# Kernel tuning notes

Hardware: AMD Instinct MI355X
Metric: run time of the kernel (lower is better)

Reference implementation:

```python
import jax, jax.numpy as jnp
import numpy as np
from jax import lax

BN_EPS = 1e-5


def _bn(t, g, b, m, v):
    # eval-mode BatchNorm2d over channel axis 1
    scale = (g / jnp.sqrt(v + BN_EPS))[None, :, None, None]
    return (t - m[None, :, None, None]) * scale + b[None, :, None, None]


def _conv1x1(t, w):
    # w: (out_c, in_c)
    return jnp.einsum('bchw,oc->bohw', t, w)


def setup_inputs() -> dict:
    key = jax.random.key(0)
    ks = jax.random.split(key, 8)
    B, C_in, H, W = 16, 640, 32, 32
    x = jax.random.normal(ks[0], (B, C_in, H, W), dtype=jnp.float32)

    def bn_params(k, c):
        k1, k2, k3, k4 = jax.random.split(k, 4)
        return (jax.random.normal(k1, (c,), jnp.float32) * 0.1 + 1.0,  # gamma
                jax.random.normal(k2, (c,), jnp.float32) * 0.1,        # beta
                jax.random.normal(k3, (c,), jnp.float32) * 0.1,        # running mean
                jax.random.uniform(k4, (c,), jnp.float32) + 0.5)       # running var

    bn1_g, bn1_b, bn1_m, bn1_v = bn_params(ks[1], 640)
    w_in = jax.random.normal(ks[2], (64, 640), jnp.float32) / np.sqrt(640)
    bnin_g, bnin_b, bnin_m, bnin_v = bn_params(ks[3], 64)
    w_emb = jax.random.normal(ks[4], (640, 1664), jnp.float32) / np.sqrt(1664)
    bne_g, bne_b, bne_m, bne_v = bn_params(ks[5], 640)
    w_out = jax.random.normal(ks[6], (640, 640), jnp.float32) / np.sqrt(640)
    bno_g, bno_b, bno_m, bno_v = bn_params(ks[7], 640)

    return dict(x=x,
                bn1_g=bn1_g, bn1_b=bn1_b, bn1_m=bn1_m, bn1_v=bn1_v,
                w_in=w_in, bnin_g=bnin_g, bnin_b=bnin_b, bnin_m=bnin_m, bnin_v=bnin_v,
                w_emb=w_emb, bne_g=bne_g, bne_b=bne_b, bne_m=bne_m, bne_v=bne_v,
                w_out=w_out, bno_g=bno_g, bno_b=bno_b, bno_m=bno_m, bno_v=bno_v)


def reference(x,
              bn1_g, bn1_b, bn1_m, bn1_v,
              w_in, bnin_g, bnin_b, bnin_m, bnin_v,
              w_emb, bne_g, bne_b, bne_m, bne_v,
              w_out, bno_g, bno_b, bno_m, bno_v):
    KH, KW = 5, 5
    x = jax.nn.relu(_bn(x, bn1_g, bn1_b, bn1_m, bn1_v))
    x = jax.nn.relu(_bn(_conv1x1(x, w_in), bnin_g, bnin_b, bnin_m, bnin_v))
    x0 = jax.nn.relu(x)  # second ReLU in original forward (no-op but faithful)
    # F.normalize(x, dim=1, p=2), eps=1e-12 (PyTorch default)
    norm = jnp.sqrt(jnp.sum(x0 * x0, axis=1, keepdims=True))
    identity = x0 / jnp.maximum(norm, 1e-12)
    b, c, h, w = identity.shape
    # unfold: (b, c*KH*KW, h, w), channel-major ordering matches torch Unfold
    patches = lax.conv_general_dilated_patches(
        identity, (KH, KW), (1, 1), ((2, 2), (2, 2)))
    corr = patches.reshape(b, c, KH * KW, h, w) * identity[:, :, None, :, :]
    corr = corr.reshape(b, c * KH * KW, h, w)
    # featureL2Norm: sqrt(sum(x^2, 1) + 1e-6)
    gs = corr / jnp.sqrt(jnp.sum(corr * corr, axis=1, keepdims=True) + 1e-6)
    feat = jnp.concatenate([identity, gs], axis=1)  # (b, 1664, h, w)
    e = jax.nn.relu(_bn(_conv1x1(feat, w_emb), bne_g, bne_b, bne_m, bne_v))
    out = _bn(_conv1x1(e, w_out), bno_g, bno_b, bno_m, bno_v)
    # dropout in eval mode = identity
    return out
```

## Files before the change

### kernel.cpp

```cpp
#include <hip/hip_runtime.h>
#include <math.h>

#define BN_EPS 1e-5f

using short8  = __attribute__((ext_vector_type(8))) short;
using f32x16  = __attribute__((ext_vector_type(16))) float;


__device__ __forceinline__ float bflo(unsigned u) { return __uint_as_float(u << 16); }
__device__ __forceinline__ float bfhi(unsigned u) { return __uint_as_float(u & 0xffff0000u); }

__device__ __forceinline__ unsigned bf16_rne(float f) {
    unsigned u = __float_as_uint(f);
    return (u + 0x7fffu + ((u >> 16) & 1u)) >> 16;
}
__device__ __forceinline__ unsigned pack_bf16(float lo, float hi) {
    return bf16_rne(lo) | (bf16_rne(hi) << 16);
}
__device__ __forceinline__ unsigned pk_hu(float lo, float hi) {
    unsigned a = __float_as_uint(lo) + 0x8000u;
    unsigned b = __float_as_uint(hi) + 0x8000u;
    return __builtin_amdgcn_perm(b, a, 0x07060302u);
}
__device__ __forceinline__ unsigned pmul_fast(unsigned a, unsigned b) {
    return pk_hu(bflo(a) * bflo(b), bfhi(a) * bfhi(b));
}

__global__ __launch_bounds__(256)
void k_prepAll(const float* __restrict__ g1, const float* __restrict__ b1,
               const float* __restrict__ m1, const float* __restrict__ v1,
               const float* __restrict__ w_in,
               const float* __restrict__ gi, const float* __restrict__ bi,
               const float* __restrict__ mi, const float* __restrict__ vi,
               const float* __restrict__ w_emb,
               const float* __restrict__ ge, const float* __restrict__ be,
               const float* __restrict__ me, const float* __restrict__ ve,
               const float* __restrict__ w_out,
               const float* __restrict__ go, const float* __restrict__ bo,
               const float* __restrict__ mo, const float* __restrict__ vo,
               float* __restrict__ s1, float* __restrict__ b1c,
               float* __restrict__ biasI, float* __restrict__ biasE, float* __restrict__ biasO,
               unsigned* __restrict__ wIt, unsigned* __restrict__ wEt, unsigned* __restrict__ wOt)
{
    __shared__ float row[1664];
    const int tid = threadIdx.x;

    if (blockIdx.x < 640) {
        const int oc = blockIdx.x;
#pragma unroll
        for (int it = 0; it < 2; it++) {
            int u = it * 256 + tid;
            if (u < 416)
                ((float4*)row)[u] = ((const float4*)&w_emb[(size_t)oc * 1664])[u];
        }
        __syncthreads();
        if (tid < 208) {
            int kc = tid >> 2, kh = (tid >> 1) & 1, ksub = tid & 1;
            int k0 = kc * 32 + kh * 16 + ksub * 8;
            float sc = ge[oc] * rsqrtf(ve[oc] + BN_EPS);
            float v[8];
#pragma unroll
            for (int j = 0; j < 8; j++) {
                int kgp = k0 + j;
                int orig;
                if (kgp < 64) orig = kgp;
                else { int t = kgp - 64; orig = 64 + (t & 63) * 25 + (t >> 6); }
                v[j] = row[orig] * sc;
            }
            int mt = oc >> 7, mf = (oc >> 5) & 3;
            int idx = (mt * 52 + kc) * 512 + (mf * 2 + kh) * 64 + ksub * 32 + (oc & 31);
            ((uint4*)wEt)[idx] = make_uint4(pack_bf16(v[0], v[1]), pack_bf16(v[2], v[3]),
                                            pack_bf16(v[4], v[5]), pack_bf16(v[6], v[7]));
        }
        return;
    }

    int i = (blockIdx.x - 640) * 256 + tid;

    if (i < 640) {
        float s = g1[i] * rsqrtf(v1[i] + BN_EPS);
        s1[i] = s; b1c[i] = b1[i] - m1[i] * s;
    } else if (i < 704) {
        int c = i - 640;
        float s = gi[c] * rsqrtf(vi[c] + BN_EPS);
        biasI[c] = bi[c] - mi[c] * s;
    } else if (i < 1344) {
        int c = i - 704;
        float s = ge[c] * rsqrtf(ve[c] + BN_EPS);
        biasE[c] = be[c] - me[c] * s;
    } else if (i < 1984) {
        int c = i - 1344;
        float s = go[c] * rsqrtf(vo[c] + BN_EPS);
        biasO[c] = bo[c] - mo[c] * s;
    }

    if (i >= 2048 && i < 7168) {
        int u = i - 2048;
        int kc = u >> 8, w = u & 255;
        int mf = w >> 7, kh = (w >> 6) & 1, sl = w & 63;
        int oc = mf * 32 + (sl & 31);
        int k0 = kc * 32 + kh * 16 + (sl >> 5) * 8;
        float sc = gi[oc] * rsqrtf(vi[oc] + BN_EPS);
        unsigned d[4];
#pragma unroll
        for (int q = 0; q < 4; q++)
            d[q] = pack_bf16(w_in[oc * 640 + k0 + 2 * q] * sc,
                             w_in[oc * 640 + k0 + 2 * q + 1] * sc);
        ((uint4*)wIt)[u] = make_uint4(d[0], d[1], d[2], d[3]);
    }

    if (i >= 8192 && i < 59392) {
        int u = i - 8192;
        int ci = u >> 9, w = u & 511;
        int mt = ci / 20, kc = ci - mt * 20;
        int mf = w >> 7, kh = (w >> 6) & 1, sl = w & 63;
        int oc = mt * 128 + mf * 32 + (sl & 31);
        int k0 = kc * 32 + kh * 16 + (sl >> 5) * 8;
        float sc = go[oc] * rsqrtf(vo[oc] + BN_EPS);
        unsigned d[4];
#pragma unroll
        for (int q = 0; q < 4; q++)
            d[q] = pack_bf16(w_out[oc * 640 + k0 + 2 * q] * sc,
                             w_out[oc * 640 + k0 + 2 * q + 1] * sc);
        ((uint4*)wOt)[u] = make_uint4(d[0], d[1], d[2], d[3]);
    }
}

__global__ __launch_bounds__(512, 1)
void k_identity(const float* __restrict__ x,
                const float* __restrict__ s1, const float* __restrict__ b1c,
                const unsigned* __restrict__ wIt, const float* __restrict__ biasI,
                unsigned* __restrict__ ident)
{
    __shared__ short smem[2][4096];
    __shared__ float Tpart[64 * 65];
    __shared__ float T[64 * 68];
    __shared__ float inv[64];

    const int tid  = threadIdx.x;
    const int half = tid >> 8;
    const int t    = tid & 255;
    const int l = t & 63, wv = t >> 6;
    const int mf = wv >> 1, nf = wv & 1;
    const int p0 = blockIdx.x * 64;
    const int b = p0 >> 10, hw0 = p0 & 1023;

    f32x16 acc;
#pragma unroll
    for (int r = 0; r < 16; r++) acc[r] = 0.f;

    for (int i = 0; i < 10; i++) {
        const int kc = half * 10 + i;
        uint4 av = ((const uint4*)wIt)[kc * 256 + t];
        int bnf = t >> 7, bkh = (t >> 6) & 1, sl = t & 63;
        int px = bnf * 32 + (sl & 31);
        int ch0 = kc * 32 + bkh * 16 + (sl >> 5) * 8;
        float4 sA = *(const float4*)&s1[ch0], sB = *(const float4*)&s1[ch0 + 4];
        float4 bA = *(const float4*)&b1c[ch0], bB = *(const float4*)&b1c[ch0 + 4];
        float vv[8];
        const float* xp = &x[((size_t)b * 640 + ch0) * 1024 + hw0 + px];
        vv[0] = fmaxf(fmaf(xp[0], sA.x, bA.x), 0.f);
        vv[1] = fmaxf(fmaf(xp[1024], sA.y, bA.y), 0.f);
        vv[2] = fmaxf(fmaf(xp[2048], sA.z, bA.z), 0.f);
        vv[3] = fmaxf(fmaf(xp[3072], sA.w, bA.w), 0.f);
        vv[4] = fmaxf(fmaf(xp[4096], sB.x, bB.x), 0.f);
        vv[5] = fmaxf(fmaf(xp[5120], sB.y, bB.y), 0.f);
        vv[6] = fmaxf(fmaf(xp[6144], sB.z, bB.z), 0.f);
        vv[7] = fmaxf(fmaf(xp[7168], sB.w, bB.w), 0.f);
        uint4 bvpk = make_uint4(pack_bf16(vv[0], vv[1]), pack_bf16(vv[2], vv[3]),
                                pack_bf16(vv[4], vv[5]), pack_bf16(vv[6], vv[7]));
        __syncthreads();
        ((uint4*)smem[half])[t] = av;
        ((uint4*)(smem[half] + 2048))[t] = bvpk;
        __syncthreads();
#pragma unroll
        for (int kh = 0; kh < 2; kh++) {
            short8 a  = *(const short8*)&smem[half][((mf * 2 + kh) * 64 + l) * 8];
            short8 bb = *(const short8*)&smem[half][2048 + ((nf * 2 + kh) * 64 + l) * 8];
            acc = __builtin_amdgcn_mfma_f32_32x32x16_bf16(a, bb, acc, 0, 0, 0);
        }
    }
    if (half == 1) {
#pragma unroll
        for (int r = 0; r < 16; r++) {
            int m = mf * 32 + (r & 3) + 8 * (r >> 2) + 4 * (l >> 5);
            int px = nf * 32 + (l & 31);
            Tpart[px * 65 + m] = acc[r];
        }
    }
    __syncthreads();
    if (half == 0) {
#pragma unroll
        for (int r = 0; r < 16; r++) {
            int m = mf * 32 + (r & 3) + 8 * (r >> 2) + 4 * (l >> 5);
            int px = nf * 32 + (l & 31);
            float v = acc[r] + Tpart[px * 65 + m];
            T[px * 68 + m] = fmaxf(v + biasI[m], 0.f);
        }
    }
    __syncthreads();
    if (tid < 64) {
        float sum = 0.f;
#pragma unroll 8
        for (int c = 0; c < 64; c++) { float v = T[tid * 68 + c]; sum = fmaf(v, v, sum); }
        inv[tid] = 1.f / fmaxf(sqrtf(sum), 1e-12f);
    }
    __syncthreads();
    {
        int px = tid >> 3, q = tid & 7;
        float iv = inv[px];
        unsigned d[4];
#pragma unroll
        for (int t2 = 0; t2 < 4; t2++)
            d[t2] = pack_bf16(T[px * 68 + q * 8 + 2 * t2] * iv,
                              T[px * 68 + q * 8 + 2 * t2 + 1] * iv);
        *(uint4*)&ident[(size_t)(p0 + px) * 32 + q * 4] = make_uint4(d[0], d[1], d[2], d[3]);
    }
}

#define FS_SLAB 0
#define FS_CTRS 15552
__global__ __launch_bounds__(512, 1)
void k_feat(const unsigned* __restrict__ ident, unsigned* __restrict__ featC, int ptBase)
{
    __shared__ short smem[20160];
    __shared__ float invDs[64];

    const int tid = threadIdx.x;
    const int pt = ptBase + blockIdx.x;
    const int b = pt >> 4, r0 = (pt & 15) * 2;

#pragma unroll
    for (int it = 0; it < 4; it++) {
        int u = it * 512 + tid;
        if (u < 1728) {
            int spx = u >> 3, q = u & 7;
            int sr = spx / 36, sc = spx - sr * 36;
            int r = r0 + sr - 2, c = sc - 2;
            uint4 v = make_uint4(0u, 0u, 0u, 0u);
            if (r >= 0 && r < 32 && c >= 0 && c < 32)
                v = *(const uint4*)&ident[((size_t)(b * 1024 + r * 32 + c) * 64 + q * 8) / 2];
            *(uint4*)&smem[FS_SLAB + spx * 72 + q * 8] = v;
        }
    }
    __syncthreads();

    {
        int px = tid >> 3, part = tid & 7;
        int rh = px >> 5, rw = px & 31;
        float ctr[8];
        const unsigned* cp = (const unsigned*)&smem[FS_SLAB + ((rh + 2) * 36 + rw + 2) * 72 + part * 8];
#pragma unroll
        for (int d = 0; d < 4; d++) { ctr[2 * d] = bflo(cp[d]); ctr[2 * d + 1] = bfhi(cp[d]); }
        float sum = 0.f;
#pragma unroll
        for (int k = 0; k < 25; k++) {
            const int kh = k / 5, kw = k % 5;
            const unsigned* nb = (const unsigned*)&smem[FS_SLAB + ((rh + kh) * 36 + rw + kw) * 72 + part * 8];
#pragma unroll
            for (int d = 0; d < 4; d++) {
                float q0 = bflo(nb[d]) * ctr[2 * d];
                float q1 = bfhi(nb[d]) * ctr[2 * d + 1];
                sum = fmaf(q0, q0, sum); sum = fmaf(q1, q1, sum);
            }
        }
        sum += __shfl_xor(sum, 1);
        sum += __shfl_xor(sum, 2);
        sum += __shfl_xor(sum, 4);
        if (part == 0) invDs[px] = rsqrtf(sum + 1e-6f);
    }
    __syncthreads();

    {
        int px = tid >> 3, q = tid & 7;
        int spx = ((px >> 5) + 2) * 36 + (px & 31) + 2;
        const unsigned* src = (const unsigned*)&smem[FS_SLAB + spx * 72 + q * 8];
        float iv = invDs[px];
        unsigned d[4];
#pragma unroll
        for (int dd = 0; dd < 4; dd++)
            d[dd] = pk_hu(bflo(src[dd]) * iv, bfhi(src[dd]) * iv);
        *(uint4*)&smem[FS_CTRS + px * 72 + q * 8] = make_uint4(d[0], d[1], d[2], d[3]);
    }
    __syncthreads();

    const int t = tid & 255;
    const int hf = t >> 7, bkh = (t >> 6) & 1, sl = t & 63;
    const int pxl = hf * 32 + (sl & 31);
    const int cl = bkh * 16 + (sl >> 5) * 8;
    const int spxC = (hf + 2) * 36 + (sl & 31) + 2;
    const int kcH = tid >> 8;
    uint4* dst = (uint4*)featC + (size_t)blockIdx.x * 52 * 256 + t;

    for (int it = 0; it < 26; it++) {
        int kc = it * 2 + kcH;
        uint4 f;
        if (kc < 2) {
            f = *(const uint4*)&smem[FS_SLAB + spxC * 72 + kc * 32 + cl];
        } else {
            int idx = kc - 2;
            int ksp = idx >> 1;
            int cb = (idx & 1) * 32 + cl;
            int kho = ksp / 5, kwo = ksp - kho * 5;
            int spx = (hf + kho) * 36 + (sl & 31) + kwo;
            const unsigned* nb = (const unsigned*)&smem[FS_SLAB + spx * 72 + cb];
            const unsigned* ct = (const unsigned*)&smem[FS_CTRS + pxl * 72 + cb];
            f = make_uint4(pmul_fast(nb[0], ct[0]), pmul_fast(nb[1], ct[1]),
                           pmul_fast(nb[2], ct[2]), pmul_fast(nb[3], ct[3]));
        }
        dst[kc * 256] = f;
    }
}

__global__ __launch_bounds__(640, 1)
void k_emb(const unsigned* __restrict__ featC, const unsigned* __restrict__ wEt,
           const float* __restrict__ biasE, unsigned* __restrict__ eG, int ntBase)
{
    __shared__ char lds[2][16384];

    const int tid = threadIdx.x;
    const int l = tid & 63;
    const int w = tid >> 6;
    const int mt = w >> 1, mf0 = (w & 1) * 2;
    const int ntL = blockIdx.x;

    const uint4* A = (const uint4*)wEt + (size_t)(mt * 52) * 512;
    const uint4* B = (const uint4*)featC + (size_t)ntL * 52 * 256;

    const int u0 = tid;
    const int u1 = tid + 640;
    const bool has2 = (tid < 384);

    f32x16 acc[2][2];
#pragma unroll
    for (int i = 0; i < 2; i++)
#pragma unroll
        for (int j = 0; j < 2; j++)
#pragma unroll
            for (int r = 0; r < 16; r++) acc[i][j][r] = 0.f;

    uint4 s0 = B[u0];
    uint4 s1;
    if (has2) s1 = B[u1];
    *(uint4*)&lds[0][u0 * 16] = s0;
    if (has2) *(uint4*)&lds[0][u1 * 16] = s1;
    __syncthreads();

    for (int c = 0; c < 13; c++) {
        const int cur = c & 1, nxt = cur ^ 1;
        if (c < 12) {
            s0 = B[(c + 1) * 1024 + u0];
            if (has2) s1 = B[(c + 1) * 1024 + u1];
        }
#pragma unroll
        for (int kcL = 0; kcL < 4; kcL++) {
            const int kc = c * 4 + kcL;
            uint4 av[2][2], bv[2][2];
#pragma unroll
            for (int mi = 0; mi < 2; mi++)
#pragma unroll
                for (int kh = 0; kh < 2; kh++)
                    av[mi][kh] = A[(size_t)kc * 512 + (((mf0 + mi) * 2 + kh) << 6) + l];
#pragma unroll
            for (int ni = 0; ni < 2; ni++)
#pragma unroll
                for (int kh = 0; kh < 2; kh++)
                    bv[ni][kh] = *(const uint4*)&lds[cur][(kcL * 256 + (ni << 7) + (kh << 6) + l) * 16];
#pragma unroll
            for (int kh = 0; kh < 2; kh++) {
                acc[0][0] = __builtin_amdgcn_mfma_f32_32x32x16_bf16(*(short8*)&av[0][kh], *(short8*)&bv[0][kh], acc[0][0], 0, 0, 0);
                acc[0][1] = __builtin_amdgcn_mfma_f32_32x32x16_bf16(*(short8*)&av[0][kh], *(short8*)&bv[1][kh], acc[0][1], 0, 0, 0);
                acc[1][0] = __builtin_amdgcn_mfma_f32_32x32x16_bf16(*(short8*)&av[1][kh], *(short8*)&bv[0][kh], acc[1][0], 0, 0, 0);
                acc[1][1] = __builtin_amdgcn_mfma_f32_32x32x16_bf16(*(short8*)&av[1][kh], *(short8*)&bv[1][kh], acc[1][1], 0, 0, 0);
            }
        }
        if (c < 12) {
            *(uint4*)&lds[nxt][u0 * 16] = s0;
            if (has2) *(uint4*)&lds[nxt][u1 * 16] = s1;
        }
        __syncthreads();
    }

    const int ptg = ntBase + ntL;
#pragma unroll
    for (int mi = 0; mi < 2; mi++) {
        const size_t kbase = ((size_t)ptg * 20 + (w * 2 + mi)) * 256;
#pragma unroll
        for (int ni = 0; ni < 2; ni++) {
#pragma unroll
            for (int rg = 0; rg < 4; rg++) {
                int ocb = w * 64 + mi * 32 + 8 * rg + 4 * (l >> 5);
                float4 bb = *(const float4*)&biasE[ocb];
                unsigned d0 = pack_bf16(fmaxf(acc[mi][ni][rg * 4 + 0] + bb.x, 0.f),
                                        fmaxf(acc[mi][ni][rg * 4 + 1] + bb.y, 0.f));
                unsigned d1 = pack_bf16(fmaxf(acc[mi][ni][rg * 4 + 2] + bb.z, 0.f),
                                        fmaxf(acc[mi][ni][rg * 4 + 3] + bb.w, 0.f));
                size_t unit = kbase + (ni << 7) + ((rg >> 1) << 6) + ((rg & 1) << 5) + (l & 31);
                ((uint2*)eG)[unit * 2 + (l >> 5)] = make_uint2(d0, d1);
            }
        }
    }
}

__global__ __launch_bounds__(640, 1)
void k_out(const unsigned* __restrict__ eG, const unsigned* __restrict__ wOt,
           const float* __restrict__ biasO, float* __restrict__ out)
{
    __shared__ char lds[2][16384];

    const int tid = threadIdx.x;
    const int l = tid & 63;
    const int w = tid >> 6;
    const int mt = w >> 1, mf0 = (w & 1) * 2;
    const int nt = blockIdx.x;
    const int p0 = nt * 64;
    const int b = p0 >> 10, hw0 = p0 & 1023;

    const uint4* A = (const uint4*)wOt + (size_t)(mt * 20) * 512;
    const uint4* B = (const uint4*)eG + (size_t)nt * 20 * 256;

    const int u0 = tid;
    const int u1 = tid + 640;
    const bool has2 = (tid < 384);

    f32x16 acc[2][2];
#pragma unroll
    for (int i = 0; i < 2; i++)
#pragma unroll
        for (int j = 0; j < 2; j++)
#pragma unroll
            for (int r = 0; r < 16; r++) acc[i][j][r] = 0.f;

    uint4 s0 = B[u0];
    uint4 s1;
    if (has2) s1 = B[u1];
    *(uint4*)&lds[0][u0 * 16] = s0;
    if (has2) *(uint4*)&lds[0][u1 * 16] = s1;
    __syncthreads();

    for (int c = 0; c < 5; c++) {
        const int cur = c & 1, nxt = cur ^ 1;
        if (c < 4) {
            s0 = B[(c + 1) * 1024 + u0];
            if (has2) s1 = B[(c + 1) * 1024 + u1];
        }
#pragma unroll
        for (int kcL = 0; kcL < 4; kcL++) {
            const int kc = c * 4 + kcL;
            uint4 av[2][2], bv[2][2];
#pragma unroll
            for (int mi = 0; mi < 2; mi++)
#pragma unroll
                for (int kh = 0; kh < 2; kh++)
                    av[mi][kh] = A[(size_t)kc * 512 + (((mf0 + mi) * 2 + kh) << 6) + l];
#pragma unroll
            for (int ni = 0; ni < 2; ni++)
#pragma unroll
                for (int kh = 0; kh < 2; kh++)
                    bv[ni][kh] = *(const uint4*)&lds[cur][(kcL * 256 + (ni << 7) + (kh << 6) + l) * 16];
#pragma unroll
            for (int kh = 0; kh < 2; kh++) {
                acc[0][0] = __builtin_amdgcn_mfma_f32_32x32x16_bf16(*(short8*)&av[0][kh], *(short8*)&bv[0][kh], acc[0][0], 0, 0, 0);
                acc[0][1] = __builtin_amdgcn_mfma_f32_32x32x16_bf16(*(short8*)&av[0][kh], *(short8*)&bv[1][kh], acc[0][1], 0, 0, 0);
                acc[1][0] = __builtin_amdgcn_mfma_f32_32x32x16_bf16(*(short8*)&av[1][kh], *(short8*)&bv[0][kh], acc[1][0], 0, 0, 0);
                acc[1][1] = __builtin_amdgcn_mfma_f32_32x32x16_bf16(*(short8*)&av[1][kh], *(short8*)&bv[1][kh], acc[1][1], 0, 0, 0);
            }
        }
        if (c < 4) {
            *(uint4*)&lds[nxt][u0 * 16] = s0;
            if (has2) *(uint4*)&lds[nxt][u1 * 16] = s1;
        }
        __syncthreads();
    }

#pragma unroll
    for (int mi = 0; mi < 2; mi++)
#pragma unroll
        for (int ni = 0; ni < 2; ni++) {
            int pxl = ni * 32 + (l & 31);
#pragma unroll
            for (int r = 0; r < 16; r++) {
                int oc = w * 64 + mi * 32 + (r & 3) + 8 * (r >> 2) + 4 * (l >> 5);
                out[((size_t)b * 640 + oc) * 1024 + hw0 + pxl] = acc[mi][ni][r] + biasO[oc];
            }
        }
}

extern "C" void kernel_launch(void* const* d_in, const int* in_sizes, int n_in,
                              void* d_out, int out_size, void* d_ws, size_t ws_size,
                              hipStream_t stream)
{
    const float* x    = (const float*)d_in[0];
    const float* g1   = (const float*)d_in[1];
    const float* b1   = (const float*)d_in[2];
    const float* m1   = (const float*)d_in[3];
    const float* v1   = (const float*)d_in[4];
    const float* w_in = (const float*)d_in[5];
    const float* gi   = (const float*)d_in[6];
    const float* bi   = (const float*)d_in[7];
    const float* mi   = (const float*)d_in[8];
    const float* vi   = (const float*)d_in[9];
    const float* w_emb= (const float*)d_in[10];
    const float* ge   = (const float*)d_in[11];
    const float* be   = (const float*)d_in[12];
    const float* me   = (const float*)d_in[13];
    const float* ve   = (const float*)d_in[14];
    const float* w_out= (const float*)d_in[15];
    const float* go   = (const float*)d_in[16];
    const float* bo   = (const float*)d_in[17];
    const float* mo   = (const float*)d_in[18];
    const float* vo   = (const float*)d_in[19];

    char* ws = (char*)d_ws;
    float*    s1    = (float*)(ws + 0);
    float*    b1c   = (float*)(ws + 2560);
    float*    biasI = (float*)(ws + 5120);
    float*    biasE = (float*)(ws + 5376);
    float*    biasO = (float*)(ws + 7936);
    unsigned* wIt   = (unsigned*)(ws + 16384);
    unsigned* wOt   = (unsigned*)(ws + 98304);
    unsigned* wEt   = (unsigned*)(ws + 917504);
    unsigned* ident = (unsigned*)(ws + 3047424);
    unsigned* eG    = (unsigned*)(ws + 5144576);
    float*    out   = (float*)d_out;

    const size_t featFullOff = 26116096ull;
    const size_t featFullBytes = 256ull * 52 * 256 * 16;

    k_prepAll<<<872, 256, 0, stream>>>(g1, b1, m1, v1, w_in, gi, bi, mi, vi,
                                       w_emb, ge, be, me, ve, w_out, go, bo, mo, vo,
                                       s1, b1c, biasI, biasE, biasO, wIt, wEt, wOt);
    k_identity<<<256, 512, 0, stream>>>(x, s1, b1c, wIt, biasI, ident);

    if (ws_size >= featFullOff + featFullBytes) {
        unsigned* featC = (unsigned*)(ws + featFullOff);
        k_feat<<<256, 512, 0, stream>>>(ident, featC, 0);
        k_emb<<<256, 640, 0, stream>>>(featC, wEt, biasE, eG, 0);
    } else {
        unsigned* featC = (unsigned*)(ws + 16384);
        for (int c = 0; c < 64; c++) {
            k_feat<<<4, 512, 0, stream>>>(ident, featC, c * 4);
            k_emb<<<4, 640, 0, stream>>>(featC, wEt, biasE, eG, c * 4);
        }
        k_prepAll<<<872, 256, 0, stream>>>(g1, b1, m1, v1, w_in, gi, bi, mi, vi,
                                           w_emb, ge, be, me, ve, w_out, go, bo, mo, vo,
                                           s1, b1c, biasI, biasE, biasO, wIt, wEt, wOt);
    }
    k_out<<<256, 640, 0, stream>>>(eG, wOt, biasO, out);
}
```

Before: 218.6 us.

## Fuse embedding and output GEMMs into one kernel via shared-memory intermediate

Merges k_emb and k_out into a single kernel. Each block's ReLU'd bf16 embedding tile stays in LDS (80 KB) and feeds the output GEMM directly, instead of round-tripping through global memory and a second launch. Launch bounds are raised to 3 blocks per CU, and the featC workspace is moved to a lower offset. The extra LDS may limit occupancy, and the second GEMM loses its global prefetch double-buffering.

```diff
diff --git a/kernel.cpp b/kernel.cpp
--- a/kernel.cpp
+++ b/kernel.cpp
@@ -312,11 +312,14 @@
     }
 }
 
-__global__ __launch_bounds__(640, 1)
-void k_emb(const unsigned* __restrict__ featC, const unsigned* __restrict__ wEt,
-           const float* __restrict__ biasE, unsigned* __restrict__ eG, int ntBase)
+__global__ __launch_bounds__(640, 3)
+void k_embout(const unsigned* __restrict__ featC, const unsigned* __restrict__ wEt,
+              const float* __restrict__ biasE,
+              const unsigned* __restrict__ wOt, const float* __restrict__ biasO,
+              float* __restrict__ out, int ntBase)
 {
     __shared__ char lds[2][16384];
+    __shared__ uint4 Ep[20 * 256];
 
     const int tid = threadIdx.x;
     const int l = tid & 63;
@@ -381,10 +384,9 @@
         __syncthreads();
     }
 
-    const int ptg = ntBase + ntL;
 #pragma unroll
     for (int mi = 0; mi < 2; mi++) {
-        const size_t kbase = ((size_t)ptg * 20 + (w * 2 + mi)) * 256;
+        const int kbase = (w * 2 + mi) * 256;
 #pragma unroll
         for (int ni = 0; ni < 2; ni++) {
 #pragma unroll
@@ -395,82 +397,46 @@
                                         fmaxf(acc[mi][ni][rg * 4 + 1] + bb.y, 0.f));
                 unsigned d1 = pack_bf16(fmaxf(acc[mi][ni][rg * 4 + 2] + bb.z, 0.f),
                                         fmaxf(acc[mi][ni][rg * 4 + 3] + bb.w, 0.f));
-                size_t unit = kbase + (ni << 7) + ((rg >> 1) << 6) + ((rg & 1) << 5) + (l & 31);
-                ((uint2*)eG)[unit * 2 + (l >> 5)] = make_uint2(d0, d1);
+                int unit = kbase + (ni << 7) + ((rg >> 1) << 6) + ((rg & 1) << 5) + (l & 31);
+                ((uint2*)Ep)[unit * 2 + (l >> 5)] = make_uint2(d0, d1);
             }
         }
     }
-}
-
-__global__ __launch_bounds__(640, 1)
-void k_out(const unsigned* __restrict__ eG, const unsigned* __restrict__ wOt,
-           const float* __restrict__ biasO, float* __restrict__ out)
-{
-    __shared__ char lds[2][16384];
-
-    const int tid = threadIdx.x;
-    const int l = tid & 63;
-    const int w = tid >> 6;
-    const int mt = w >> 1, mf0 = (w & 1) * 2;
-    const int nt = blockIdx.x;
+    __syncthreads();
+
+    const int nt = ntBase + ntL;
     const int p0 = nt * 64;
     const int b = p0 >> 10, hw0 = p0 & 1023;
-
-    const uint4* A = (const uint4*)wOt + (size_t)(mt * 20) * 512;
-    const uint4* B = (const uint4*)eG + (size_t)nt * 20 * 256;
-
-    const int u0 = tid;
-    const int u1 = tid + 640;
-    const bool has2 = (tid < 384);
-
-    f32x16 acc[2][2];
+    const uint4* Ao = (const uint4*)wOt + (size_t)(mt * 20) * 512;
+
+    f32x16 acc2[2][2];
 #pragma unroll
     for (int i = 0; i < 2; i++)
 #pragma unroll
         for (int j = 0; j < 2; j++)
 #pragma unroll
-            for (int r = 0; r < 16; r++) acc[i][j][r] = 0.f;
-
-    uint4 s0 = B[u0];
-    uint4 s1;
-    if (has2) s1 = B[u1];
-    *(uint4*)&lds[0][u0 * 16] = s0;
-    if (has2) *(uint4*)&lds[0][u1 * 16] = s1;
-    __syncthreads();
-
-    for (int c = 0; c < 5; c++) {
-        const int cur = c & 1, nxt = cur ^ 1;
-        if (c < 4) {
-            s0 = B[(c + 1) * 1024 + u0];
-            if (has2) s1 = B[(c + 1) * 1024 + u1];
-        }
-#pragma unroll
-        for (int kcL = 0; kcL < 4; kcL++) {
-            const int kc = c * 4 + kcL;
-            uint4 av[2][2], bv[2][2];
-#pragma unroll
-            for (int mi = 0; mi < 2; mi++)
-#pragma unroll
-                for (int kh = 0; kh < 2; kh++)
-                    av[mi][kh] = A[(size_t)kc * 512 + (((mf0 + mi) * 2 + kh) << 6) + l];
-#pragma unroll
-            for (int ni = 0; ni < 2; ni++)
-#pragma unroll
-                for (int kh = 0; kh < 2; kh++)
-                    bv[ni][kh] = *(const uint4*)&lds[cur][(kcL * 256 + (ni << 7) + (kh << 6) + l) * 16];
-#pragma unroll
-            for (int kh = 0; kh < 2; kh++) {
-                acc[0][0] = __builtin_amdgcn_mfma_f32_32x32x16_bf16(*(short8*)&av[0][kh], *(short8*)&bv[0][kh], acc[0][0], 0, 0, 0);
-                acc[0][1] = __builtin_amdgcn_mfma_f32_32x32x16_bf16(*(short8*)&av[0][kh], *(short8*)&bv[1][kh], acc[0][1], 0, 0, 0);
-                acc[1][0] = __builtin_amdgcn_mfma_f32_32x32x16_bf16(*(short8*)&av[1][kh], *(short8*)&bv[0][kh], acc[1][0], 0, 0, 0);
-                acc[1][1] = __builtin_amdgcn_mfma_f32_32x32x16_bf16(*(short8*)&av[1][kh], *(short8*)&bv[1][kh], acc[1][1], 0, 0, 0);
-            }
-        }
-        if (c < 4) {
-            *(uint4*)&lds[nxt][u0 * 16] = s0;
-            if (has2) *(uint4*)&lds[nxt][u1 * 16] = s1;
-        }
-        __syncthreads();
+            for (int r = 0; r < 16; r++) acc2[i][j][r] = 0.f;
+
+#pragma unroll 2
+    for (int kc = 0; kc < 20; kc++) {
+        uint4 av[2][2], bv[2][2];
+#pragma unroll
+        for (int mi = 0; mi < 2; mi++)
+#pragma unroll
+            for (int kh = 0; kh < 2; kh++)
+                av[mi][kh] = Ao[(size_t)kc * 512 + (((mf0 + mi) * 2 + kh) << 6) + l];
+#pragma unroll
+        for (int ni = 0; ni < 2; ni++)
+#pragma unroll
+            for (int kh = 0; kh < 2; kh++)
+                bv[ni][kh] = Ep[kc * 256 + (ni << 7) + (kh << 6) + l];
+#pragma unroll
+        for (int kh = 0; kh < 2; kh++) {
+            acc2[0][0] = __builtin_amdgcn_mfma_f32_32x32x16_bf16(*(short8*)&av[0][kh], *(short8*)&bv[0][kh], acc2[0][0], 0, 0, 0);
+            acc2[0][1] = __builtin_amdgcn_mfma_f32_32x32x16_bf16(*(short8*)&av[0][kh], *(short8*)&bv[1][kh], acc2[0][1], 0, 0, 0);
+            acc2[1][0] = __builtin_amdgcn_mfma_f32_32x32x16_bf16(*(short8*)&av[1][kh], *(short8*)&bv[0][kh], acc2[1][0], 0, 0, 0);
+            acc2[1][1] = __builtin_amdgcn_mfma_f32_32x32x16_bf16(*(short8*)&av[1][kh], *(short8*)&bv[1][kh], acc2[1][1], 0, 0, 0);
+        }
     }
 
 #pragma unroll
@@ -481,7 +447,7 @@
 #pragma unroll
             for (int r = 0; r < 16; r++) {
                 int oc = w * 64 + mi * 32 + (r & 3) + 8 * (r >> 2) + 4 * (l >> 5);
-                out[((size_t)b * 640 + oc) * 1024 + hw0 + pxl] = acc[mi][ni][r] + biasO[oc];
+                out[((size_t)b * 640 + oc) * 1024 + hw0 + pxl] = acc2[mi][ni][r] + biasO[oc];
             }
         }
 }
@@ -521,30 +487,24 @@
     unsigned* wOt   = (unsigned*)(ws + 98304);
     unsigned* wEt   = (unsigned*)(ws + 917504);
     unsigned* ident = (unsigned*)(ws + 3047424);
-    unsigned* eG    = (unsigned*)(ws + 5144576);
+    unsigned* featC = (unsigned*)(ws + 5144576);
     float*    out   = (float*)d_out;
 
-    const size_t featFullOff = 26116096ull;
     const size_t featFullBytes = 256ull * 52 * 256 * 16;
+    const size_t featFullEnd   = 5144576ull + featFullBytes;
 
     k_prepAll<<<872, 256, 0, stream>>>(g1, b1, m1, v1, w_in, gi, bi, mi, vi,
                                        w_emb, ge, be, me, ve, w_out, go, bo, mo, vo,
                                        s1, b1c, biasI, biasE, biasO, wIt, wEt, wOt);
     k_identity<<<256, 512, 0, stream>>>(x, s1, b1c, wIt, biasI, ident);
 
-    if (ws_size >= featFullOff + featFullBytes) {
-        unsigned* featC = (unsigned*)(ws + featFullOff);
+    if (ws_size >= featFullEnd) {
         k_feat<<<256, 512, 0, stream>>>(ident, featC, 0);
-        k_emb<<<256, 640, 0, stream>>>(featC, wEt, biasE, eG, 0);
+        k_embout<<<256, 640, 0, stream>>>(featC, wEt, biasE, wOt, biasO, out, 0);
     } else {
-        unsigned* featC = (unsigned*)(ws + 16384);
         for (int c = 0; c < 64; c++) {
             k_feat<<<4, 512, 0, stream>>>(ident, featC, c * 4);
-            k_emb<<<4, 640, 0, stream>>>(featC, wEt, biasE, eG, c * 4);
-        }
-        k_prepAll<<<872, 256, 0, stream>>>(g1, b1, m1, v1, w_in, gi, bi, mi, vi,
-                                           w_emb, ge, be, me, ve, w_out, go, bo, mo, vo,
-                                           s1, b1c, biasI, biasE, biasO, wIt, wEt, wOt);
-    }
-    k_out<<<256, 640, 0, stream>>>(eG, wOt, biasO, out);
-}
+            k_embout<<<4, 640, 0, stream>>>(featC, wEt, biasE, wOt, biasO, out, c * 4);
+        }
+    }
+}
```

After: 208.2 us. -4.8%, faster.
